# Kernel tuning notes

Hardware: AMD Instinct MI355X
Metric: run time of the kernel (lower is better)

The kernel has to match this reference:

```python
import jax, jax.numpy as jnp
import numpy as np

B, T, D, H = 4, 2048, 1024, 16
HD = D // H
EPS = 1e-5
NEG = 1e10


def setup_inputs() -> dict:
    key = jax.random.key(0)
    k1, k2, k3 = jax.random.split(key, 3)
    return {
        "target": jax.random.normal(k1, (B, T, D), dtype=jnp.float32),
        "w_qkv": jax.random.normal(k2, (D, 3 * D), dtype=jnp.float32) * 0.02,
        "w_proj": jax.random.normal(k3, (D, D), dtype=jnp.float32) * (0.02 / np.sqrt(24.0)),
        "b_proj": jnp.zeros((D,), dtype=jnp.float32),
        "ln_gamma": jnp.ones((D,), dtype=jnp.float32),
        "ln_beta": jnp.zeros((D,), dtype=jnp.float32),
    }


def reference(target, w_qkv, w_proj, b_proj, ln_gamma, ln_beta):
    b, t, d = target.shape
    resid = target
    qkv = target @ w_qkv                      # [B,T,3D]
    q, k, v = jnp.split(qkv, 3, axis=-1)
    # [B,H,T,hd]
    q = q.reshape(b, t, H, HD).transpose(0, 2, 1, 3)
    k = k.reshape(b, t, H, HD).transpose(0, 2, 1, 3)
    v = v.reshape(b, t, H, HD).transpose(0, 2, 1, 3)
    scores = jnp.einsum("bhqd,bhkd->bhqk", q, k) * (1.0 / np.sqrt(HD))
    causal = (jnp.arange(t)[:, None] >= jnp.arange(t)[None, :]).astype(scores.dtype)
    scores = scores * causal - (1.0 - causal) * NEG
    attn = jax.nn.softmax(scores, axis=-1)
    out = jnp.einsum("bhqk,bhkd->bhqd", attn, v)
    out = out.transpose(0, 2, 1, 3).reshape(b, t, d)
    proj = out @ w_proj + b_proj
    x = proj + resid
    mu = jnp.mean(x, axis=-1, keepdims=True)
    var = jnp.var(x, axis=-1, keepdims=True)
    return ((x - mu) * jax.lax.rsqrt(var + EPS)) * ln_gamma + ln_beta
```

## Files before the change

kernel.cpp:

```cpp
#include <hip/hip_runtime.h>
#include <hip/hip_bf16.h>

#define Bsz 4
#define Tseq 2048
#define Dmodel 1024
#define Hn 16
#define HD 64
#define EPS 1e-5f
#define QSCALE 0.18033688011112042f

typedef __attribute__((ext_vector_type(8))) short bf16x8;
typedef __attribute__((ext_vector_type(4))) short bf16x4;
typedef __attribute__((ext_vector_type(4))) float f32x4;
typedef __attribute__((ext_vector_type(4))) unsigned short us4;
typedef __attribute__((ext_vector_type(2))) unsigned uint2v;

typedef const __attribute__((address_space(1))) void* gas_t;
typedef __attribute__((address_space(3))) void* las_t;

__device__ __forceinline__ unsigned short f2bf(float x) {
    unsigned u = __builtin_bit_cast(unsigned, x);
    u += 0x7fffu + ((u >> 16) & 1u);
    return (unsigned short)(u >> 16);
}
__device__ __forceinline__ unsigned pack2bf_t(float a, float b) {
    return (__builtin_bit_cast(unsigned, a) >> 16)
         | (__builtin_bit_cast(unsigned, b) & 0xffff0000u);
}

__device__ __forceinline__ f32x4 mfma16x16x16(bf16x4 a, bf16x4 b, f32x4 c) {
#if __has_builtin(__builtin_amdgcn_mfma_f32_16x16x16bf16_1k)
    return __builtin_amdgcn_mfma_f32_16x16x16bf16_1k(a, b, c, 0, 0, 0);
#else
    asm("v_mfma_f32_16x16x16_bf16 %0, %1, %2, %0" : "+v"(c) : "v"(a), "v"(b));
    return c;
#endif
}

__global__ void cast_bf16(const float* __restrict__ in, unsigned short* __restrict__ out) {
    int i = (blockIdx.x * 256 + threadIdx.x) * 4;
    float4 v = *(const float4*)(in + i);
    us4 o = { f2bf(v.x), f2bf(v.y), f2bf(v.z), f2bf(v.w) };
    *(us4*)(out + i) = o;
}

__global__ void transpose_cast(const float* __restrict__ in, unsigned short* __restrict__ out,
                               int K, int N) {
    __shared__ unsigned short t[32][33];
    int k0 = blockIdx.y * 32, n0 = blockIdx.x * 32;
    int tx = threadIdx.x, ty = threadIdx.y;
    #pragma unroll
    for (int i = 0; i < 32; i += 8)
        t[ty + i][tx] = f2bf(in[(size_t)(k0 + ty + i) * N + n0 + tx]);
    __syncthreads();
    #pragma unroll
    for (int i = 0; i < 32; i += 8)
        out[(size_t)(n0 + ty + i) * K + k0 + tx] = t[tx][ty + i];
}

template<bool OUT_BF16, bool SCALEQ>
__global__ __launch_bounds__(256)
void gemm_mfma(const unsigned short* __restrict__ A,
               const unsigned short* __restrict__ Bt,
               void* __restrict__ Cv, int M, int N, int K,
               const float* __restrict__ bias, const float* __restrict__ resid) {
    __shared__ unsigned short As[128 * 32];
    __shared__ unsigned short Bs[128 * 32];
    const int tid = threadIdx.x;
    const int w = tid >> 6, lane = tid & 63;
    const int l16 = lane & 15, quad = lane >> 4;

    const int lin = blockIdx.y * gridDim.x + blockIdx.x;
    const int chunk = (gridDim.x * gridDim.y) >> 3;
    const int neff = (lin & 7) * chunk + (lin >> 3);
    const int bx = neff % gridDim.x, by = neff / gridDim.x;
    const int m0 = by * 128, n0 = bx * 128;

    f32x4 acc[4][4];
    #pragma unroll
    for (int i = 0; i < 4; ++i)
        #pragma unroll
        for (int j = 0; j < 4; ++j)
            acc[i][j] = f32x4{0.f, 0.f, 0.f, 0.f};

    const int lrow = lane >> 2, lcol = lane & 3;
    const unsigned short* ag = A  + (size_t)(m0 + w * 32 + lrow) * K + lcol * 8;
    const unsigned short* bg = Bt + (size_t)(n0 + w * 32 + lrow) * K + lcol * 8;
    unsigned short* al0 = As + (w * 32) * 32;
    unsigned short* al1 = As + (w * 32 + 16) * 32;
    unsigned short* bl0 = Bs + (w * 32) * 32;
    unsigned short* bl1 = Bs + (w * 32 + 16) * 32;
    const int am = (w >> 1) * 64, bn = (w & 1) * 64;

    for (int k0 = 0; k0 < K; k0 += 32) {
        __builtin_amdgcn_global_load_lds((gas_t)(ag + k0),          (las_t)al0, 16, 0, 0);
        __builtin_amdgcn_global_load_lds((gas_t)(ag + 16 * K + k0), (las_t)al1, 16, 0, 0);
        __builtin_amdgcn_global_load_lds((gas_t)(bg + k0),          (las_t)bl0, 16, 0, 0);
        __builtin_amdgcn_global_load_lds((gas_t)(bg + 16 * K + k0), (las_t)bl1, 16, 0, 0);
        __syncthreads();

        bf16x8 af[4], bf[4];
        #pragma unroll
        for (int i = 0; i < 4; ++i)
            af[i] = *(const bf16x8*)&As[(am + i * 16 + l16) * 32 + quad * 8];
        #pragma unroll
        for (int j = 0; j < 4; ++j)
            bf[j] = *(const bf16x8*)&Bs[(bn + j * 16 + l16) * 32 + quad * 8];
        #pragma unroll
        for (int i = 0; i < 4; ++i)
            #pragma unroll
            for (int j = 0; j < 4; ++j)
                acc[i][j] = __builtin_amdgcn_mfma_f32_16x16x32_bf16(af[i], bf[j], acc[i][j], 0, 0, 0);
        __syncthreads();
    }

    #pragma unroll
    for (int i = 0; i < 4; ++i) {
        #pragma unroll
        for (int j = 0; j < 4; ++j) {
            const int col = n0 + bn + j * 16 + l16;
            const float scale = (SCALEQ && col < Dmodel) ? QSCALE : 1.0f;
            #pragma unroll
            for (int r = 0; r < 4; ++r) {
                const int row = m0 + am + i * 16 + quad * 4 + r;
                if (OUT_BF16) {
                    ((unsigned short*)Cv)[(size_t)row * N + col] = f2bf(acc[i][j][r] * scale);
                } else {
                    float v = acc[i][j][r] + bias[col] + resid[(size_t)row * N + col];
                    ((float*)Cv)[(size_t)row * N + col] = v;
                }
            }
        }
    }
}

__global__ __launch_bounds__(256)
void flash_attn(const unsigned short* __restrict__ qkv, unsigned short* __restrict__ out) {
    const int lin = blockIdx.y * gridDim.x + blockIdx.x;
    const int xcd = lin & 7, local = lin >> 3;
    const int bh = xcd + 8 * (local & 7);
    const int x = local >> 3;
    const int qt_lo = x, qt_hi = (Tseq / 64 - 1) - x;
    const int h = bh & (Hn - 1), b = bh >> 4;
    const int tid = threadIdx.x;
    const int wave = tid >> 6;
    const int lane = tid & 63;
    const int l16 = lane & 15;
    const int quad = lane >> 4;

    __shared__ unsigned short Ks[2][2][64 * 32];
    __shared__ unsigned short Vs[2][64 * 64];

    const unsigned short* qrow = qkv + ((size_t)(b * Tseq + wave * 16 + l16)) * 3072 + h * HD;
    const unsigned short* qhi = qrow + (size_t)qt_hi * 64 * 3072;
    const unsigned short* qlo = qrow + (size_t)qt_lo * 64 * 3072;
    bf16x8 qh0 = *(const bf16x8*)(qhi + quad * 8);
    bf16x8 qh1 = *(const bf16x8*)(qhi + 32 + quad * 8);
    bf16x8 ql0 = *(const bf16x8*)(qlo + quad * 8);
    bf16x8 ql1 = *(const bf16x8*)(qlo + 32 + quad * 8);

    float l_hi = 0.f, l_lo = 0.f;
    f32x4 ohi[4], olo[4];
    #pragma unroll
    for (int nt = 0; nt < 4; ++nt) {
        ohi[nt] = f32x4{0.f, 0.f, 0.f, 0.f};
        olo[nt] = f32x4{0.f, 0.f, 0.f, 0.f};
    }

    const unsigned short* kbase = qkv + (size_t)b * Tseq * 3072 + Dmodel + h * HD;
    const unsigned short* vbase = kbase + Dmodel;
    const unsigned short* kg = kbase + (size_t)(wave * 16 + (lane >> 2)) * 3072 + (lane & 3) * 8;
    const int vp = tid >> 3, vc = tid & 7;
    const unsigned short* vsrc = vbase + (size_t)(2 * vp) * 3072 + vc * 8;

    auto stageK = [&](int buf, size_t koff) {
        __builtin_amdgcn_global_load_lds((gas_t)(kg + koff),
                                         (las_t)&Ks[buf][0][wave * 16 * 32], 16, 0, 0);
        __builtin_amdgcn_global_load_lds((gas_t)(kg + koff + 32),
                                         (las_t)&Ks[buf][1][wave * 16 * 32], 16, 0, 0);
    };
    auto writeV = [&](int buf, const bf16x8& va, const bf16x8& vb) {
        const int kc = vp >> 2;
        const int kin = (2 * vp) & 7;
        #pragma unroll
        for (int j = 0; j < 8; ++j) {
            const int d = vc * 8 + j;
            const int pc = kc ^ ((d + (d >> 3)) & 7);
            unsigned pk = (unsigned)(unsigned short)va[j]
                        | ((unsigned)(unsigned short)vb[j] << 16);
            *(unsigned*)&Vs[buf][d * 64 + pc * 8 + kin] = pk;
        }
    };

    auto compute = [&](int buf, int q0t, const bf16x8& qf0, const bf16x8& qf1,
                       f32x4* oacc, float& l_part, bool diag, int k0g) {
        __builtin_amdgcn_s_setprio(1);
        f32x4 st[4];
        #pragma unroll
        for (int nt = 0; nt < 4; ++nt) {
            f32x4 a = {0.f, 0.f, 0.f, 0.f};
            bf16x8 kf0 = *(const bf16x8*)&Ks[buf][0][(nt * 16 + l16) * 32 + quad * 8];
            a = __builtin_amdgcn_mfma_f32_16x16x32_bf16(kf0, qf0, a, 0, 0, 0);
            bf16x8 kf1 = *(const bf16x8*)&Ks[buf][1][(nt * 16 + l16) * 32 + quad * 8];
            a = __builtin_amdgcn_mfma_f32_16x16x32_bf16(kf1, qf1, a, 0, 0, 0);
            st[nt] = a;
        }
        if (diag) {
            const int qg = q0t + wave * 16 + l16;
            #pragma unroll
            for (int nt = 0; nt < 4; ++nt) {
                const int kgl = k0g + nt * 16 + quad * 4;
                #pragma unroll
                for (int r = 0; r < 4; ++r)
                    if (kgl + r > qg) st[nt][r] = -1e30f;
            }
        }
        bf16x4 pa[4];
        #pragma unroll
        for (int nt = 0; nt < 4; ++nt) {
            float p0 = exp2f(st[nt][0]);
            float p1 = exp2f(st[nt][1]);
            float p2 = exp2f(st[nt][2]);
            float p3 = exp2f(st[nt][3]);
            l_part += (p0 + p1) + (p2 + p3);
            uint2v t;
            t.x = pack2bf_t(p0, p1);
            t.y = pack2bf_t(p2, p3);
            pa[nt] = __builtin_bit_cast(bf16x4, t);
        }
        #pragma unroll
        for (int ntk = 0; ntk < 4; ++ntk) {
            const int k0 = ntk * 16 + quad * 4;
            const int chunk = k0 >> 3;
            const int kin = k0 & 7;
            #pragma unroll
            for (int ntd = 0; ntd < 4; ++ntd) {
                const int d = ntd * 16 + l16;
                const int pc = chunk ^ ((d + (d >> 3)) & 7);
                bf16x4 vf = *(const bf16x4*)&Vs[buf][d * 64 + pc * 8 + kin];
                oacc[ntd] = mfma16x16x16(pa[ntk], vf, oacc[ntd]);
            }
        }
        __builtin_amdgcn_s_setprio(0);
    };

    stageK(0, 0);
    bf16x8 va = *(const bf16x8*)(vsrc);
    bf16x8 vb = *(const bf16x8*)(vsrc + 3072);
    writeV(0, va, vb);
    __syncthreads();

    int cur = 0;
    for (int kt = 0; kt <= qt_hi; ++kt) {
        if (kt < qt_hi) {
            const size_t koff_n = (size_t)(kt + 1) * 64 * 3072;
            stageK(cur ^ 1, koff_n);
            va = *(const bf16x8*)(vsrc + koff_n);
            vb = *(const bf16x8*)(vsrc + koff_n + 3072);
        }

        compute(cur, qt_hi * 64, qh0, qh1, ohi, l_hi, kt == qt_hi, kt * 64);
        if (kt <= qt_lo)
            compute(cur, qt_lo * 64, ql0, ql1, olo, l_lo, kt == qt_lo, kt * 64);

        if (kt < qt_hi) writeV(cur ^ 1, va, vb);
        __syncthreads();
        cur ^= 1;
    }

    auto epilogue = [&](int q0t, f32x4* oacc, float l_part) {
        l_part += __shfl_xor(l_part, 16, 64);
        l_part += __shfl_xor(l_part, 32, 64);
        float inv[4];
        #pragma unroll
        for (int r = 0; r < 4; ++r) {
            float lr = __shfl(l_part, quad * 4 + r, 64);
            inv[r] = __builtin_amdgcn_rcpf(lr);
        }
        unsigned short* obase =
            out + ((size_t)(b * Tseq + q0t + wave * 16)) * Dmodel + h * HD;
        #pragma unroll
        for (int nt = 0; nt < 4; ++nt) {
            #pragma unroll
            for (int r = 0; r < 4; ++r) {
                int row = quad * 4 + r;
                obase[(size_t)row * Dmodel + nt * 16 + l16] = f2bf(oacc[nt][r] * inv[r]);
            }
        }
    };
    epilogue(qt_hi * 64, ohi, l_hi);
    epilogue(qt_lo * 64, olo, l_lo);
}

__global__ void ln_kernel(float* __restrict__ x, const float* __restrict__ gamma,
                          const float* __restrict__ beta) {
    const int row = blockIdx.x;
    float* xr = x + (size_t)row * Dmodel;
    const int tid = threadIdx.x;
    __shared__ float rs[256], rs2[256];

    float4 v = *(const float4*)(xr + tid * 4);
    float s  = v.x + v.y + v.z + v.w;
    float s2 = v.x * v.x + v.y * v.y + v.z * v.z + v.w * v.w;
    rs[tid] = s; rs2[tid] = s2;
    __syncthreads();
    for (int off = 128; off; off >>= 1) {
        if (tid < off) { rs[tid] += rs[tid + off]; rs2[tid] += rs2[tid + off]; }
        __syncthreads();
    }
    const float mu  = rs[0] * (1.0f / Dmodel);
    const float var = rs2[0] * (1.0f / Dmodel) - mu * mu;
    const float rstd = rsqrtf(var + EPS);

    float4 g = *(const float4*)(gamma + tid * 4);
    float4 bt = *(const float4*)(beta + tid * 4);
    float4 o;
    o.x = (v.x - mu) * rstd * g.x + bt.x;
    o.y = (v.y - mu) * rstd * g.y + bt.y;
    o.z = (v.z - mu) * rstd * g.z + bt.z;
    o.w = (v.w - mu) * rstd * g.w + bt.w;
    *(float4*)(xr + tid * 4) = o;
}

extern "C" void kernel_launch(void* const* d_in, const int* in_sizes, int n_in,
                              void* d_out, int out_size, void* d_ws, size_t ws_size,
                              hipStream_t stream) {
    const float* target   = (const float*)d_in[0];
    const float* w_qkv    = (const float*)d_in[1];
    const float* w_proj   = (const float*)d_in[2];
    const float* b_proj   = (const float*)d_in[3];
    const float* ln_gamma = (const float*)d_in[4];
    const float* ln_beta  = (const float*)d_in[5];
    float* out = (float*)d_out;

    const int M = Bsz * Tseq;

    char* ws = (char*)d_ws;
    unsigned short* qkv_bf16 = (unsigned short*)(ws);
    unsigned short* attn_bf  = (unsigned short*)(ws + 48ull * 1024 * 1024);
    unsigned short* tgt_bf   = (unsigned short*)(ws + 64ull * 1024 * 1024);
    unsigned short* wqT      = (unsigned short*)(ws + 80ull * 1024 * 1024);
    unsigned short* wpT      = (unsigned short*)(ws + 86ull * 1024 * 1024);

    cast_bf16<<<dim3(M * Dmodel / 1024), 256, 0, stream>>>(target, tgt_bf);
    transpose_cast<<<dim3(3072 / 32, Dmodel / 32), dim3(32, 8), 0, stream>>>(
        w_qkv, wqT, Dmodel, 3072);
    transpose_cast<<<dim3(Dmodel / 32, Dmodel / 32), dim3(32, 8), 0, stream>>>(
        w_proj, wpT, Dmodel, Dmodel);

    gemm_mfma<true, true><<<dim3(3072 / 128, M / 128), 256, 0, stream>>>(
        tgt_bf, wqT, qkv_bf16, M, 3072, Dmodel, nullptr, nullptr);

    flash_attn<<<dim3(Tseq / 128, Bsz * Hn), 256, 0, stream>>>(qkv_bf16, attn_bf);

    gemm_mfma<false, false><<<dim3(Dmodel / 128, M / 128), 256, 0, stream>>>(
        attn_bf, wpT, out, M, Dmodel, Dmodel, b_proj, target);

    ln_kernel<<<dim3(M), 256, 0, stream>>>(out, ln_gamma, ln_beta);
}
```

Baseline: 295.7 us.

## Process four causal query tiles per attention block to share K/V loads

Each attention workgroup now handles four query tiles (x, 15-x, 16+x, 31-x) instead of two, so every staged K/V tile in LDS is reused by up to four query tiles. The grid shrinks from 16 to 8 blocks per head, halving K/V global traffic per head while keeping causal work balanced across blocks. The cost is more accumulator and Q registers per thread, which may lower occupancy, and fewer total workgroups (512) to fill the GPU. The bf16 pack helper also now uses a single v_perm byte permute instead of shift/mask/or.

```diff
diff --git a/kernel.cpp b/kernel.cpp
--- a/kernel.cpp
+++ b/kernel.cpp
@@ -24,8 +24,8 @@
     return (unsigned short)(u >> 16);
 }
 __device__ __forceinline__ unsigned pack2bf_t(float a, float b) {
-    return (__builtin_bit_cast(unsigned, a) >> 16)
-         | (__builtin_bit_cast(unsigned, b) & 0xffff0000u);
+    return __builtin_amdgcn_perm(__builtin_bit_cast(unsigned, b),
+                                 __builtin_bit_cast(unsigned, a), 0x07060302u);
 }
 
 __device__ __forceinline__ f32x4 mfma16x16x16(bf16x4 a, bf16x4 b, f32x4 c) {
@@ -140,7 +140,7 @@
     const int xcd = lin & 7, local = lin >> 3;
     const int bh = xcd + 8 * (local & 7);
     const int x = local >> 3;
-    const int qt_lo = x, qt_hi = (Tseq / 64 - 1) - x;
+    const int t0 = x, t1 = 15 - x, t2 = 16 + x, t3 = 31 - x;
     const int h = bh & (Hn - 1), b = bh >> 4;
     const int tid = threadIdx.x;
     const int wave = tid >> 6;
@@ -152,19 +152,23 @@
     __shared__ unsigned short Vs[2][64 * 64];
 
     const unsigned short* qrow = qkv + ((size_t)(b * Tseq + wave * 16 + l16)) * 3072 + h * HD;
-    const unsigned short* qhi = qrow + (size_t)qt_hi * 64 * 3072;
-    const unsigned short* qlo = qrow + (size_t)qt_lo * 64 * 3072;
-    bf16x8 qh0 = *(const bf16x8*)(qhi + quad * 8);
-    bf16x8 qh1 = *(const bf16x8*)(qhi + 32 + quad * 8);
-    bf16x8 ql0 = *(const bf16x8*)(qlo + quad * 8);
-    bf16x8 ql1 = *(const bf16x8*)(qlo + 32 + quad * 8);
-
-    float l_hi = 0.f, l_lo = 0.f;
-    f32x4 ohi[4], olo[4];
+    bf16x8 q0a, q0b, q1a, q1b, q2a, q2b, q3a, q3b;
+    {
+        const unsigned short* q;
+        q = qrow + (size_t)t0 * 64 * 3072; q0a = *(const bf16x8*)(q + quad * 8); q0b = *(const bf16x8*)(q + 32 + quad * 8);
+        q = qrow + (size_t)t1 * 64 * 3072; q1a = *(const bf16x8*)(q + quad * 8); q1b = *(const bf16x8*)(q + 32 + quad * 8);
+        q = qrow + (size_t)t2 * 64 * 3072; q2a = *(const bf16x8*)(q + quad * 8); q2b = *(const bf16x8*)(q + 32 + quad * 8);
+        q = qrow + (size_t)t3 * 64 * 3072; q3a = *(const bf16x8*)(q + quad * 8); q3b = *(const bf16x8*)(q + 32 + quad * 8);
+    }
+
+    float l0 = 0.f, l1 = 0.f, l2 = 0.f, l3 = 0.f;
+    f32x4 o0[4], o1[4], o2[4], o3[4];
     #pragma unroll
     for (int nt = 0; nt < 4; ++nt) {
-        ohi[nt] = f32x4{0.f, 0.f, 0.f, 0.f};
-        olo[nt] = f32x4{0.f, 0.f, 0.f, 0.f};
+        o0[nt] = f32x4{0.f, 0.f, 0.f, 0.f};
+        o1[nt] = f32x4{0.f, 0.f, 0.f, 0.f};
+        o2[nt] = f32x4{0.f, 0.f, 0.f, 0.f};
+        o3[nt] = f32x4{0.f, 0.f, 0.f, 0.f};
     }
 
     const unsigned short* kbase = qkv + (size_t)b * Tseq * 3072 + Dmodel + h * HD;
@@ -251,19 +255,20 @@
     __syncthreads();
 
     int cur = 0;
-    for (int kt = 0; kt <= qt_hi; ++kt) {
-        if (kt < qt_hi) {
+    for (int kt = 0; kt <= t3; ++kt) {
+        if (kt < t3) {
             const size_t koff_n = (size_t)(kt + 1) * 64 * 3072;
             stageK(cur ^ 1, koff_n);
             va = *(const bf16x8*)(vsrc + koff_n);
             vb = *(const bf16x8*)(vsrc + koff_n + 3072);
         }
 
-        compute(cur, qt_hi * 64, qh0, qh1, ohi, l_hi, kt == qt_hi, kt * 64);
-        if (kt <= qt_lo)
-            compute(cur, qt_lo * 64, ql0, ql1, olo, l_lo, kt == qt_lo, kt * 64);
-
-        if (kt < qt_hi) writeV(cur ^ 1, va, vb);
+        compute(cur, t3 * 64, q3a, q3b, o3, l3, kt == t3, kt * 64);
+        if (kt <= t2) compute(cur, t2 * 64, q2a, q2b, o2, l2, kt == t2, kt * 64);
+        if (kt <= t1) compute(cur, t1 * 64, q1a, q1b, o1, l1, kt == t1, kt * 64);
+        if (kt <= t0) compute(cur, t0 * 64, q0a, q0b, o0, l0, kt == t0, kt * 64);
+
+        if (kt < t3) writeV(cur ^ 1, va, vb);
         __syncthreads();
         cur ^= 1;
     }
@@ -288,8 +293,10 @@
             }
         }
     };
-    epilogue(qt_hi * 64, ohi, l_hi);
-    epilogue(qt_lo * 64, olo, l_lo);
+    epilogue(t3 * 64, o3, l3);
+    epilogue(t2 * 64, o2, l2);
+    epilogue(t1 * 64, o1, l1);
+    epilogue(t0 * 64, o0, l0);
 }
 
 __global__ void ln_kernel(float* __restrict__ x, const float* __restrict__ gamma,
@@ -351,7 +358,7 @@
     gemm_mfma<true, true><<<dim3(3072 / 128, M / 128), 256, 0, stream>>>(
         tgt_bf, wqT, qkv_bf16, M, 3072, Dmodel, nullptr, nullptr);
 
-    flash_attn<<<dim3(Tseq / 128, Bsz * Hn), 256, 0, stream>>>(qkv_bf16, attn_bf);
+    flash_attn<<<dim3(8, Bsz * Hn), 256, 0, stream>>>(qkv_bf16, attn_bf);
 
     gemm_mfma<false, false><<<dim3(Dmodel / 128, M / 128), 256, 0, stream>>>(
         attn_bf, wpT, out, M, Dmodel, Dmodel, b_proj, target);
```

After: 323.2 us. 9.3% more time.
